# Performance work log

Hardware: AMD Instinct MI355X
Metric: run time of the kernel (lower is better)

The kernel has to match this reference:

```python
import jax, jax.numpy as jnp
import numpy as np

DIM = 768
HEADS = 12
HEAD_DIM = DIM // HEADS
WS = 14  # window size
MLP = 3072
EPS = 1e-6
SCALE = HEAD_DIM ** -0.5
B, H, W = 4, 64, 64


def setup_inputs() -> dict:
    key = jax.random.key(0)
    ks = jax.random.split(key, 8)
    s = 0.02
    f32 = jnp.float32
    return {
        "hidden_states": jax.random.normal(ks[0], (B, DIM, H, W), f32),
        "ln1_w": jnp.ones((DIM,), f32),
        "ln1_b": jnp.zeros((DIM,), f32),
        "qkv_w": jax.random.normal(ks[1], (DIM, 3 * DIM), f32) * s,
        "qkv_b": jnp.zeros((3 * DIM,), f32),
        "proj_w": jax.random.normal(ks[2], (DIM, DIM), f32) * s,
        "proj_b": jnp.zeros((DIM,), f32),
        "rel_pos_h": jax.random.normal(ks[3], (2 * WS - 1, HEAD_DIM), f32) * s,
        "rel_pos_w": jax.random.normal(ks[4], (2 * WS - 1, HEAD_DIM), f32) * s,
        "ln2_w": jnp.ones((DIM,), f32),
        "ln2_b": jnp.zeros((DIM,), f32),
        "fc1_w": jax.random.normal(ks[5], (DIM, MLP), f32) * s,
        "fc1_b": jnp.zeros((MLP,), f32),
        "fc2_w": jax.random.normal(ks[6], (MLP, DIM), f32) * s,
        "fc2_b": jnp.zeros((DIM,), f32),
    }


def _layer_norm(x, w, b):
    mu = jnp.mean(x, axis=-1, keepdims=True)
    var = jnp.mean(jnp.square(x - mu), axis=-1, keepdims=True)
    return (x - mu) * jax.lax.rsqrt(var + EPS) * w + b


def _get_rel_pos(size, rel_pos):
    # q_size == k_size == WS, rel_pos already has 2*WS-1 rows -> pure gather
    coords = jnp.arange(size)[:, None] - jnp.arange(size)[None, :] + (size - 1)
    return rel_pos[coords]  # (size, size, head_dim)


def _attention(x, qkv_w, qkv_b, proj_w, proj_b, rel_pos_h, rel_pos_w):
    nb, h, w, c = x.shape  # windows batch, WS, WS, DIM
    n = h * w
    qkv = x.reshape(nb, n, c) @ qkv_w + qkv_b  # (nb, n, 3*DIM)
    qkv = qkv.reshape(nb, n, 3, HEADS, HEAD_DIM).transpose(2, 0, 3, 1, 4)
    qkv = qkv.reshape(3, nb * HEADS, n, HEAD_DIM)
    q, k, v = qkv[0], qkv[1], qkv[2]
    attn = jnp.einsum('bqc,bkc->bqk', q * SCALE, k)  # (nb*HEADS, n, n)
    # decomposed relative position bias
    Rh = _get_rel_pos(h, rel_pos_h)  # (h, h, hd)
    Rw = _get_rel_pos(w, rel_pos_w)  # (w, w, hd)
    rq = q.reshape(-1, h, w, HEAD_DIM)
    rel_h = jnp.einsum('bhwc,hkc->bhwk', rq, Rh)
    rel_w = jnp.einsum('bhwc,wkc->bhwk', rq, Rw)
    attn = (attn.reshape(-1, h, w, h, w)
            + rel_h[:, :, :, :, None]
            + rel_w[:, :, :, None, :]).reshape(-1, n, n)
    attn = jax.nn.softmax(attn, axis=-1)
    out = attn @ v  # (nb*HEADS, n, hd)
    out = out.reshape(nb, HEADS, h, w, HEAD_DIM).transpose(0, 2, 3, 1, 4)
    out = out.reshape(nb, h, w, c)
    return out @ proj_w + proj_b


def reference(hidden_states, ln1_w, ln1_b, qkv_w, qkv_b, proj_w, proj_b,
              rel_pos_h, rel_pos_w, ln2_w, ln2_b, fc1_w, fc1_b, fc2_w, fc2_b):
    x = hidden_states.transpose(0, 2, 3, 1)  # NCHW -> NHWC
    b, h, w, c = x.shape
    shortcut = x
    x = _layer_norm(x, ln1_w, ln1_b)
    # window partition with padding
    ph = (WS - h % WS) % WS
    pw = (WS - w % WS) % WS
    x = jnp.pad(x, ((0, 0), (0, ph), (0, pw), (0, 0)))
    hp, wp = h + ph, w + pw
    x = x.reshape(b, hp // WS, WS, wp // WS, WS, c).transpose(0, 1, 3, 2, 4, 5)
    windows = x.reshape(-1, WS, WS, c)
    windows = _attention(windows, qkv_w, qkv_b, proj_w, proj_b, rel_pos_h, rel_pos_w)
    # window unpartition + crop
    x = windows.reshape(b, hp // WS, wp // WS, WS, WS, c).transpose(0, 1, 3, 2, 4, 5)
    x = x.reshape(b, hp, wp, c)[:, :h, :w, :]
    x = shortcut + x
    y = _layer_norm(x, ln2_w, ln2_b)
    y = jax.nn.gelu(y @ fc1_w + fc1_b, approximate=False) @ fc2_w + fc2_b
    x = x + y
    return x.transpose(0, 3, 1, 2)  # back to NCHW
```

## Files before the change

### kernel.cpp

```cpp
#include <hip/hip_runtime.h>
#include <cstdint>
#include <cstddef>

#define NIMG   4
#define GRIDSZ 64
#define CH     768
#define NHEAD  12
#define WSZ    14
#define NWINS  100
#define NTOK   196
#define MWIN   19600
#define MREAL  16384
#define MLPC   3072
#define QKSCALE 0.125f

#define KSTR 72
#define VSTR 216
#define PSTR 40

typedef unsigned short u16;
typedef __attribute__((ext_vector_type(8))) short bf16x8;
typedef __attribute__((ext_vector_type(4))) float f32x4;

__device__ __forceinline__ float b2f(u16 u) {
  uint32_t x = (uint32_t)u << 16; float f; __builtin_memcpy(&f, &x, 4); return f;
}
__device__ __forceinline__ u16 f2b(float f) {
  uint32_t x; __builtin_memcpy(&x, &f, 4);
  x += 0x7fffu + ((x >> 16) & 1u);
  return (u16)(x >> 16);
}

__device__ __forceinline__ float fast_gelu(float x) {
  float z  = x * 0.70710678118654752440f;
  float az = fabsf(z);
  float t  = 1.0f / (1.0f + 0.3275911f * az);
  float poly = ((((1.061405429f * t - 1.453152027f) * t + 1.421413741f) * t
                 - 0.284496736f) * t + 0.254829592f) * t;
  float e  = __expf(-az * az);
  float erfv = copysignf(1.0f - poly * e, z);
  return 0.5f * x * (1.0f + erfv);
}

__device__ __forceinline__ void gl_lds16(const u16* g, u16* l) {
  __builtin_amdgcn_global_load_lds(
      (const __attribute__((address_space(1))) unsigned int*)g,
      (__attribute__((address_space(3))) unsigned int*)l, 16, 0, 0);
}

__global__ __launch_bounds__(256) void k_nchw2nhwc(const float* __restrict__ in,
                                                   float* __restrict__ out) {
  __shared__ float tile[32][33];
  int b  = blockIdx.z;
  int g0 = blockIdx.x * 32;
  int c0 = blockIdx.y * 32;
  int tx = threadIdx.x, ty = threadIdx.y;
  const float* ip = in + (size_t)b * CH * 4096;
  float* op = out + (size_t)b * 4096 * CH;
#pragma unroll
  for (int k = 0; k < 32; k += 8)
    tile[ty + k][tx] = ip[(size_t)(c0 + ty + k) * 4096 + g0 + tx];
  __syncthreads();
#pragma unroll
  for (int k = 0; k < 32; k += 8)
    op[(size_t)(g0 + ty + k) * CH + c0 + tx] = tile[tx][ty + k];
}

__global__ __launch_bounds__(256) void k_nhwc2nchw(const float* __restrict__ in,
                                                   float* __restrict__ out) {
  __shared__ float tile[32][33];
  int b  = blockIdx.z;
  int g0 = blockIdx.x * 32;
  int c0 = blockIdx.y * 32;
  int tx = threadIdx.x, ty = threadIdx.y;
  const float* ip = in + (size_t)b * 4096 * CH;
  float* op = out + (size_t)b * CH * 4096;
#pragma unroll
  for (int k = 0; k < 32; k += 8)
    tile[ty + k][tx] = ip[(size_t)(g0 + ty + k) * CH + c0 + tx];
  __syncthreads();
#pragma unroll
  for (int k = 0; k < 32; k += 8)
    op[(size_t)(c0 + ty + k) * 4096 + g0 + tx] = tile[tx][ty + k];
}

__global__ __launch_bounds__(256) void k_wt(const float* __restrict__ in,
                                            u16* __restrict__ out,
                                            int K, int N) {
  __shared__ float t[32][33];
  int n0 = blockIdx.x * 32, k0 = blockIdx.y * 32;
  int tx = threadIdx.x, ty = threadIdx.y;
#pragma unroll
  for (int k = 0; k < 32; k += 8)
    t[ty + k][tx] = in[(size_t)(k0 + ty + k) * N + n0 + tx];
  __syncthreads();
#pragma unroll
  for (int k = 0; k < 32; k += 8)
    out[(size_t)(n0 + ty + k) * K + k0 + tx] = f2b(t[tx][ty + k]);
}

__global__ __launch_bounds__(256) void k_ln(const float* __restrict__ x,
                                            const float* __restrict__ wt,
                                            const float* __restrict__ bs,
                                            u16* __restrict__ y,
                                            int window_mode) {
  int wid = threadIdx.x >> 6, lane = threadIdx.x & 63;
  int row = blockIdx.x * 4 + wid;
  const float* xp = x + (size_t)row * CH;
  float v[12];
#pragma unroll
  for (int k = 0; k < 6; k++) {
    float2 f2 = *(const float2*)&xp[k * 128 + lane * 2];
    v[2 * k] = f2.x; v[2 * k + 1] = f2.y;
  }
  float s = 0.f;
#pragma unroll
  for (int k = 0; k < 12; k++) s += v[k];
#pragma unroll
  for (int off = 32; off > 0; off >>= 1) s += __shfl_xor(s, off, 64);
  float mu = s * (1.0f / 768.0f);
  float vs = 0.f;
#pragma unroll
  for (int k = 0; k < 12; k++) { float d = v[k] - mu; vs += d * d; }
#pragma unroll
  for (int off = 32; off > 0; off >>= 1) vs += __shfl_xor(vs, off, 64);
  float rs = rsqrtf(vs * (1.0f / 768.0f) + 1e-6f);
  int orow = row;
  if (window_mode) {
    int b = row >> 12, hw = row & 4095;
    int h = hw >> 6, wc = hw & 63;
    orow = (b * 25 + (h / WSZ) * 5 + (wc / WSZ)) * NTOK + (h % WSZ) * WSZ + (wc % WSZ);
  }
  u16* yp = y + (size_t)orow * CH;
#pragma unroll
  for (int k = 0; k < 6; k++) {
    int c = k * 128 + lane * 2;
    float2 w2 = *(const float2*)&wt[c];
    float2 b2 = *(const float2*)&bs[c];
    ushort2 st = make_ushort2(f2b((v[2 * k] - mu) * rs * w2.x + b2.x),
                              f2b((v[2 * k + 1] - mu) * rs * w2.y + b2.y));
    *(ushort2*)&yp[c] = st;
  }
}

__device__ __forceinline__ void gemm_epilogue_row(
    const f32x4* accrow, int row, int colbase, int N,
    const float* __restrict__ bias, void* __restrict__ Cv,
    u16* __restrict__ Vt, int act, int mode, int row0, int M) {
  if (row >= M) return;
  size_t gbase = 0;
  bool valid = true;
  int wloc = 0, tok = 0;
  if (mode == 2) {
    int rowa = row + row0;
    int widx = rowa / NTOK, tt = rowa % NTOK;
    int b = widx / 25, wq = widx % 25;
    int h = (wq / 5) * WSZ + tt / WSZ;
    int w = (wq % 5) * WSZ + tt % WSZ;
    valid = (h < GRIDSZ) && (w < GRIDSZ);
    gbase = valid ? ((size_t)((b * GRIDSZ + h) * GRIDSZ + w)) * CH : 0;
  }
  if (mode == 3) { wloc = row / NTOK; tok = row - wloc * NTOK; }
#pragma unroll
  for (int ni = 0; ni < 4; ni++) {
    int colb = colbase + ni * 16;
    float4 b4 = *(const float4*)&bias[colb];
    float v[4] = {accrow[ni][0] + b4.x, accrow[ni][1] + b4.y,
                  accrow[ni][2] + b4.z, accrow[ni][3] + b4.w};
    if (act == 1) {
#pragma unroll
      for (int r2 = 0; r2 < 4; r2++) v[r2] = fast_gelu(v[r2]);
    }
    if (mode == 0) {
      ushort4 st = make_ushort4(f2b(v[0]), f2b(v[1]), f2b(v[2]), f2b(v[3]));
      *(ushort4*)((u16*)Cv + (size_t)row * N + colb) = st;
    } else if (mode == 1) {
      float4* p = (float4*)((float*)Cv + (size_t)row * N + colb);
      float4 o = *p;
      o.x += v[0]; o.y += v[1]; o.z += v[2]; o.w += v[3];
      *p = o;
    } else if (mode == 2) {
      if (valid) {
        float4* p = (float4*)((float*)Cv + gbase + colb);
        float4 o = *p;
        o.x += v[0]; o.y += v[1]; o.z += v[2]; o.w += v[3];
        *p = o;
      }
    } else {
      if (colb < 1536) {
        ushort4 st = make_ushort4(f2b(v[0]), f2b(v[1]), f2b(v[2]), f2b(v[3]));
        *(ushort4*)((u16*)Cv + (size_t)row * N + colb) = st;
      } else {
        int vv = colb - 1536, hd = vv >> 6, d = vv & 63;
        u16* vp = Vt + ((size_t)(wloc * NHEAD + hd) * 64 + d) * VSTR + tok;
#pragma unroll
        for (int r2 = 0; r2 < 4; r2++) vp[(size_t)r2 * VSTR] = f2b(v[r2]);
      }
    }
  }
}

__global__ __launch_bounds__(256, 3) void k_gemm_mfma(const u16* __restrict__ A,
                                                      const u16* __restrict__ BT,
                                                      const float* __restrict__ bias,
                                                      void* __restrict__ Cv,
                                                      u16* __restrict__ Vt,
                                                      int M, int N, int K,
                                                      int act, int mode, int row0) {
  __shared__ u16 As[3][128 * 32];
  __shared__ u16 Bs[3][128 * 32];
  int tid  = threadIdx.x;
  int lane = tid & 63, wave = tid >> 6;

  int gx   = gridDim.x, gy = gridDim.y;
  int nwg  = gx * gy;
  int orig = blockIdx.y * gx + blockIdx.x;
  int q = nwg >> 3, r = nwg & 7;
  int xcd = orig & 7, idx = orig >> 3;
  int wgid = (xcd < r ? xcd * (q + 1) : r * (q + 1) + (xcd - r) * q) + idx;

  int GM = 3145728 / (128 * K * 2);
  if (GM < 2) GM = 2;
  if (GM > gy) GM = gy;
  int gsz   = GM * gx;
  int grp   = wgid / gsz;
  int first = grp * GM;
  int gm    = gy - first; if (gm > GM) gm = GM;
  int loc   = wgid - grp * gsz;
  int bm    = first + loc % gm;
  int bn    = loc / gm;

  int wm = (wave & 1) * 64, wn = (wave >> 1) * 64;
  int l15 = lane & 15, quad = lane >> 4;
  int xq = (quad ^ ((l15 >> 1) & 3)) * 8;

  f32x4 acc[4][4];
#pragma unroll
  for (int i = 0; i < 4; i++)
#pragma unroll
    for (int j = 0; j < 4; j++) acc[i][j] = (f32x4){0.f, 0.f, 0.f, 0.f};

  const u16* Atile = A + (size_t)bm * 128 * K;
  const u16* Btile = BT + (size_t)bn * 128 * K;

  const u16* ga[2];
  const u16* gb[2];
#pragma unroll
  for (int i = 0; i < 2; ++i) {
    int c_ = i * 256 + wave * 64 + lane;
    int row_ = c_ >> 2, gs_ = (c_ & 3) ^ ((c_ >> 3) & 3);
    ga[i] = Atile + (size_t)row_ * K + gs_ * 8;
    gb[i] = Btile + (size_t)row_ * K + gs_ * 8;
  }

  const int nk = K >> 5;

#define STAGE(slot)                                                          \
  do {                                                                       \
    _Pragma("unroll")                                                        \
    for (int i = 0; i < 2; ++i) {                                            \
      gl_lds16(ga[i], &As[(slot)][(i * 256 + wave * 64) * 8]);               \
      ga[i] += 32;                                                           \
      gl_lds16(gb[i], &Bs[(slot)][(i * 256 + wave * 64) * 8]);               \
      gb[i] += 32;                                                           \
    }                                                                        \
  } while (0)

#define COMPUTE(slot)                                                        \
  do {                                                                       \
    bf16x8 af[4], bfv[4];                                                    \
    _Pragma("unroll")                                                        \
    for (int mi = 0; mi < 4; mi++)                                           \
      af[mi] = *(const bf16x8*)&As[(slot)][(wm + mi * 16 + l15) * 32 + xq];  \
    _Pragma("unroll")                                                        \
    for (int ni = 0; ni < 4; ni++)                                           \
      bfv[ni] = *(const bf16x8*)&Bs[(slot)][(wn + ni * 16 + l15) * 32 + xq]; \
    _Pragma("unroll")                                                        \
    for (int mi = 0; mi < 4; mi++)                                           \
      _Pragma("unroll")                                                      \
      for (int ni = 0; ni < 4; ni++)                                         \
        acc[mi][ni] = __builtin_amdgcn_mfma_f32_16x16x32_bf16(               \
            bfv[ni], af[mi], acc[mi][ni], 0, 0, 0);                          \
  } while (0)

#define WAITL                                                                \
  do {                                                                       \
    asm volatile("s_waitcnt vmcnt(4)" ::: "memory");                         \
    __builtin_amdgcn_s_barrier();                                            \
  } while (0)

  STAGE(0);
  STAGE(1);

  for (int g = 0; g < nk - 3; g += 3) {
    WAITL; STAGE(2); COMPUTE(0);
    WAITL; STAGE(0); COMPUTE(1);
    WAITL; STAGE(1); COMPUTE(2);
  }
  WAITL; STAGE(2); COMPUTE(0);
  WAITL;           COMPUTE(1);
  asm volatile("s_waitcnt vmcnt(0)" ::: "memory");
  __builtin_amdgcn_s_barrier();
  COMPUTE(2);

#undef STAGE
#undef COMPUTE
#undef WAITL

#pragma unroll
  for (int mi = 0; mi < 4; mi++) {
    int row = bm * 128 + wm + mi * 16 + l15;
    int colbase = bn * 128 + wn + quad * 4;
    gemm_epilogue_row(acc[mi], row, colbase, N, bias, Cv, Vt, act, mode, row0, M);
  }
}

__global__ __launch_bounds__(256) void k_relbias(const u16* __restrict__ qkv,
                                                 const float* __restrict__ rel_h,
                                                 const float* __restrict__ rel_w,
                                                 u16* __restrict__ rhg,
                                                 u16* __restrict__ rwg,
                                                 int nrows) {
  int idx = blockIdx.x * 256 + threadIdx.x;
  if (idx >= nrows * NHEAD) return;
  int head = idx % NHEAD, row = idx / NHEAD;
  int wloc = row / NTOK, tok = row - wloc * NTOK;
  const u16* qp = qkv + (size_t)row * (3 * CH) + head * 64;
  float q[64];
#pragma unroll
  for (int d = 0; d < 64; d += 4) {
    ushort4 u4 = *(const ushort4*)(qp + d);
    q[d] = b2f(u4.x); q[d + 1] = b2f(u4.y); q[d + 2] = b2f(u4.z); q[d + 3] = b2f(u4.w);
  }
  int hq = tok / WSZ, wq = tok % WSZ;
  size_t obase = ((size_t)(wloc * NHEAD + head) * NTOK + tok) * 16;
  for (int kk = 0; kk < WSZ; kk++) {
    const float* rh = rel_h + (size_t)(hq - kk + WSZ - 1) * 64;
    const float* rw = rel_w + (size_t)(wq - kk + WSZ - 1) * 64;
    float sh = 0.0f, sw = 0.0f;
#pragma unroll
    for (int d = 0; d < 64; d++) { sh += q[d] * rh[d]; sw += q[d] * rw[d]; }
    rhg[obase + kk] = f2b(sh);
    rwg[obase + kk] = f2b(sw);
  }
}

__global__ __launch_bounds__(256) void k_attn_mfma(const u16* __restrict__ qkv,
                                                   const u16* __restrict__ Vt,
                                                   const u16* __restrict__ rhg,
                                                   const u16* __restrict__ rwg,
                                                   u16* __restrict__ out,
                                                   int win0) {
  __shared__ u16 Ks[NTOK * KSTR];
  __shared__ u16 Vs[64 * VSTR];
  __shared__ u16 Ps[4][16 * PSTR];
  __shared__ u16 RhL[NTOK * 16];
  __shared__ u16 RwL[NTOK * 16];
  int head = blockIdx.x, wloc = blockIdx.y;
  int tid = threadIdx.x, lane = tid & 63, wave = tid >> 6;
  int l15 = lane & 15, quad = lane >> 4;
  const u16* qbase = qkv + (size_t)wloc * NTOK * (3 * CH) + head * 64;

  for (int c = tid; c < NTOK * 8; c += 256) {
    int tok = c >> 3, part = c & 7;
    uint4 v = *(const uint4*)(qbase + (size_t)tok * (3 * CH) + CH + part * 8);
    *(uint4*)&Ks[tok * KSTR + part * 8] = v;
  }
  {
    const uint4* rhp4 = (const uint4*)(rhg + ((size_t)(wloc * NHEAD + head) * NTOK) * 16);
    const uint4* rwp4 = (const uint4*)(rwg + ((size_t)(wloc * NHEAD + head) * NTOK) * 16);
    for (int c = tid; c < NTOK * 2; c += 256) {
      ((uint4*)RhL)[c] = rhp4[c];
      ((uint4*)RwL)[c] = rwp4[c];
    }
  }
  const u16* vb = Vt + (size_t)(wloc * NHEAD + head) * 64 * VSTR;
#pragma unroll
  for (int it = 0; it < 7; ++it) {
    int c = it * 256 + tid;
    if (c < 64 * VSTR / 8) gl_lds16(vb + (size_t)c * 8, Vs + ((size_t)it * 256 + wave * 64) * 8);
  }
  __syncthreads();

  int winabs = win0 + wloc;

  for (int t16 = wave; t16 < 13; t16 += 4) {
    int qtok = t16 * 16 + l15; if (qtok > NTOK - 1) qtok = NTOK - 1;
    bf16x8 aq0 = *(const bf16x8*)(qbase + (size_t)qtok * (3 * CH) + quad * 8);
    bf16x8 aq1 = *(const bf16x8*)(qbase + (size_t)qtok * (3 * CH) + 32 + quad * 8);

    f32x4 s[13];
#pragma unroll
    for (int ct = 0; ct < 13; ct++) s[ct] = (f32x4){0.f, 0.f, 0.f, 0.f};
#pragma unroll
    for (int ct = 0; ct < 13; ct++) {
      int ktok = ct * 16 + l15; if (ktok > NTOK - 1) ktok = NTOK - 1;
      bf16x8 bk0 = *(const bf16x8*)&Ks[ktok * KSTR + quad * 8];
      bf16x8 bk1 = *(const bf16x8*)&Ks[ktok * KSTR + 32 + quad * 8];
      s[ct] = __builtin_amdgcn_mfma_f32_16x16x32_bf16(aq0, bk0, s[ct], 0, 0, 0);
      s[ct] = __builtin_amdgcn_mfma_f32_16x16x32_bf16(aq1, bk1, s[ct], 0, 0, 0);
    }

    f32x4 o[4];
#pragma unroll
    for (int ni = 0; ni < 4; ni++) o[ni] = (f32x4){0.f, 0.f, 0.f, 0.f};
    float lsum[4] = {0.f, 0.f, 0.f, 0.f};
    int row0t = t16 * 16 + quad * 4;

#pragma unroll
    for (int cc = 0; cc < 7; ++cc) {
#pragma unroll
      for (int half = 0; half < 2; ++half) {
        int ct = cc * 2 + half;
        if (ct < 13) {
          int col = ct * 16 + l15;
          int jh = col / WSZ, jw = col - jh * WSZ;
          bool colok = col < NTOK;
#pragma unroll
          for (int r = 0; r < 4; r++) {
            int rowt = row0t + r; int rowc = rowt > NTOK - 1 ? NTOK - 1 : rowt;
            float bias = b2f(RhL[rowc * 16 + jh]) + b2f(RwL[rowc * 16 + jw]);
            float sv = s[ct][r] * QKSCALE + bias;
            float p = colok ? __expf(sv) : 0.f;
            lsum[r] += p;
            Ps[wave][(quad * 4 + r) * PSTR + half * 16 + l15] = f2b(p);
          }
        } else {
#pragma unroll
          for (int r = 0; r < 4; r++)
            Ps[wave][(quad * 4 + r) * PSTR + half * 16 + l15] = 0;
        }
      }
      bf16x8 pa = *(const bf16x8*)&Ps[wave][l15 * PSTR + quad * 8];
#pragma unroll
      for (int ni = 0; ni < 4; ni++) {
        bf16x8 bv = *(const bf16x8*)&Vs[(ni * 16 + l15) * VSTR + cc * 32 + quad * 8];
        o[ni] = __builtin_amdgcn_mfma_f32_16x16x32_bf16(pa, bv, o[ni], 0, 0, 0);
      }
    }

#pragma unroll
    for (int r = 0; r < 4; r++) {
#pragma unroll
      for (int m = 1; m < 16; m <<= 1) lsum[r] += __shfl_xor(lsum[r], m, 64);
    }

#pragma unroll
    for (int r = 0; r < 4; r++) {
      int rowt = row0t + r;
      if (rowt < NTOK) {
        float inv = 1.0f / lsum[r];
        u16* op = out + ((size_t)winabs * NTOK + rowt) * CH + head * 64;
#pragma unroll
        for (int ni = 0; ni < 4; ni++) op[ni * 16 + l15] = f2b(o[ni][r] * inv);
      }
    }
  }
}

extern "C" void kernel_launch(void* const* d_in, const int* in_sizes, int n_in,
                              void* d_out, int out_size, void* d_ws, size_t ws_size,
                              hipStream_t stream) {
  const float* hidden = (const float*)d_in[0];
  const float* ln1_w  = (const float*)d_in[1];
  const float* ln1_b  = (const float*)d_in[2];
  const float* qkv_w  = (const float*)d_in[3];
  const float* qkv_b  = (const float*)d_in[4];
  const float* proj_w = (const float*)d_in[5];
  const float* proj_b = (const float*)d_in[6];
  const float* rel_h  = (const float*)d_in[7];
  const float* rel_w  = (const float*)d_in[8];
  const float* ln2_w  = (const float*)d_in[9];
  const float* ln2_b  = (const float*)d_in[10];
  const float* fc1_w  = (const float*)d_in[11];
  const float* fc1_b  = (const float*)d_in[12];
  const float* fc2_w  = (const float*)d_in[13];
  const float* fc2_b  = (const float*)d_in[14];
  float* out = (float*)d_out;

  char* ws = (char*)d_ws;
  float* x_nhwc = (float*)ws;
  u16*   R1     = (u16*)(ws + 50331648);
  u16*   qkvT   = (u16*)(ws + 80437248);
  u16*   projT  = qkvT + (size_t)2304 * 768;
  u16*   fc1T   = projT + (size_t)768 * 768;
  u16*   fc2T   = fc1T + (size_t)3072 * 768;
  u16*   R2     = fc2T + (size_t)768 * 3072;
  size_t used   = (size_t)80437248 + 14155776;
  size_t r2e    = ws_size > used ? (ws_size - used) >> 1 : 0;

  const size_t PW_QKV = (size_t)NTOK * 3 * CH;
  const size_t PW_VT  = (size_t)NHEAD * 64 * VSTR;
  const size_t PW_RB  = (size_t)NHEAD * NTOK * 16;
  const size_t perwin = PW_QKV + PW_VT + 2 * PW_RB;
  size_t wc_s = r2e / perwin;
  int Wc = wc_s >= NWINS ? NWINS : (int)wc_s;
  if (Wc < 1) Wc = 1;
  size_t rc_s = (r2e / MLPC / 128) * 128;
  int Rc = rc_s >= MREAL ? MREAL : (int)rc_s;
  if (Rc < 128) Rc = 128;

  u16* Vt  = R2 + (size_t)Wc * PW_QKV;
  u16* rhg = Vt + (size_t)Wc * PW_VT;
  u16* rwg = rhg + (size_t)Wc * PW_RB;

  k_wt<<<dim3(72, 24), dim3(32, 8), 0, stream>>>(qkv_w, qkvT, CH, 3 * CH);
  k_wt<<<dim3(24, 24), dim3(32, 8), 0, stream>>>(proj_w, projT, CH, CH);
  k_wt<<<dim3(96, 24), dim3(32, 8), 0, stream>>>(fc1_w, fc1T, CH, MLPC);
  k_wt<<<dim3(24, 96), dim3(32, 8), 0, stream>>>(fc2_w, fc2T, MLPC, CH);

  hipMemsetAsync(R1, 0, (size_t)MWIN * CH * sizeof(u16), stream);

  k_nchw2nhwc<<<dim3(128, 24, NIMG), dim3(32, 8), 0, stream>>>(hidden, x_nhwc);
  k_ln<<<MREAL / 4, 256, 0, stream>>>(x_nhwc, ln1_w, ln1_b, R1, 1);
  for (int w0 = 0; w0 < NWINS; w0 += Wc) {
    int wc = NWINS - w0 < Wc ? NWINS - w0 : Wc;
    int Mc = wc * NTOK;
    k_gemm_mfma<<<dim3(18, (Mc + 127) / 128), 256, 0, stream>>>(
        R1 + (size_t)w0 * NTOK * CH, qkvT, qkv_b, R2, Vt,
        Mc, 3 * CH, CH, 0, 3, 0);
    k_relbias<<<(Mc * NHEAD + 255) / 256, 256, 0, stream>>>(
        R2, rel_h, rel_w, rhg, rwg, Mc);
    k_attn_mfma<<<dim3(NHEAD, wc), 256, 0, stream>>>(
        R2, Vt, rhg, rwg, R1, w0);
  }
  k_gemm_mfma<<<dim3(6, (MWIN + 127) / 128), 256, 0, stream>>>(
      R1, projT, proj_b, x_nhwc, nullptr, MWIN, CH, CH, 0, 2, 0);
  k_ln<<<MREAL / 4, 256, 0, stream>>>(x_nhwc, ln2_w, ln2_b, R1, 0);
  for (int r0 = 0; r0 < MREAL; r0 += Rc) {
    int rc = MREAL - r0 < Rc ? MREAL - r0 : Rc;
    k_gemm_mfma<<<dim3(24, (rc + 127) / 128), 256, 0, stream>>>(
        R1 + (size_t)r0 * CH, fc1T, fc1_b, R2, nullptr, rc, MLPC, CH, 1, 0, 0);
    k_gemm_mfma<<<dim3(6, (rc + 127) / 128), 256, 0, stream>>>(
        R2, fc2T, fc2_b, x_nhwc + (size_t)r0 * CH, nullptr, rc, CH, MLPC, 0, 1, 0);
  }
  k_nhwc2nchw<<<dim3(128, 24, NIMG), dim3(32, 8), 0, stream>>>(x_nhwc, out);
}
```

Before: 745.6 us.

## Add barrier-free per-wave-staged GEMM kernel for MLP fc1/fc2

Adds a new GEMM kernel in which each wave loads its own 64-row A and B slices into private LDS buffers with direct global-to-LDS copies. Wave-local data lets the double-buffered pipeline use only vmcnt/lgkmcnt waits, with no workgroup barriers. The MLP fc1 and fc2 GEMMs switch to this kernel. In exchange, A and B rows are duplicated across waves, which doubles global/L2 traffic and LDS footprint, so occupancy drops to 2 blocks per CU. The block-mapping code is moved into a shared helper.

```diff
diff --git a/kernel.cpp b/kernel.cpp
--- a/kernel.cpp
+++ b/kernel.cpp
@@ -200,6 +200,119 @@
   }
 }
 
+__device__ __forceinline__ void map_block(int K, int& bm, int& bn) {
+  int gx = gridDim.x, gy = gridDim.y;
+  int nwg = gx * gy;
+  int orig = blockIdx.y * gx + blockIdx.x;
+  int q = nwg >> 3, r = nwg & 7;
+  int xcd = orig & 7, idx = orig >> 3;
+  int wgid = (xcd < r ? xcd * (q + 1) : r * (q + 1) + (xcd - r) * q) + idx;
+  int GM = 3145728 / (128 * K * 2);
+  if (GM < 2) GM = 2;
+  if (GM > gy) GM = gy;
+  int gsz   = GM * gx;
+  int grp   = wgid / gsz;
+  int first = grp * GM;
+  int gm    = gy - first; if (gm > GM) gm = GM;
+  int loc   = wgid - grp * gsz;
+  bm = first + loc % gm;
+  bn = loc / gm;
+}
+
+__global__ __launch_bounds__(256, 2) void k_gemm_nb(const u16* __restrict__ A,
+                                                    const u16* __restrict__ BT,
+                                                    const float* __restrict__ bias,
+                                                    void* __restrict__ Cv,
+                                                    u16* __restrict__ Vt,
+                                                    int M, int N, int K,
+                                                    int act, int mode, int row0) {
+  __shared__ u16 Aw[4][2][64 * 32];
+  __shared__ u16 Bw[4][2][64 * 32];
+  int tid  = threadIdx.x;
+  int lane = tid & 63, wave = tid >> 6;
+
+  int bm, bn;
+  map_block(K, bm, bn);
+
+  int wm = (wave & 1) * 64, wn = (wave >> 1) * 64;
+  int l15 = lane & 15, quad = lane >> 4;
+  int xq = (quad ^ ((l15 >> 1) & 3)) * 8;
+
+  f32x4 acc[4][4];
+#pragma unroll
+  for (int i = 0; i < 4; i++)
+#pragma unroll
+    for (int j = 0; j < 4; j++) acc[i][j] = (f32x4){0.f, 0.f, 0.f, 0.f};
+
+  const u16* Atile = A + (size_t)(bm * 128 + wm) * K;
+  const u16* Btile = BT + (size_t)(bn * 128 + wn) * K;
+
+  const u16* ga[4];
+  const u16* gb[4];
+#pragma unroll
+  for (int i = 0; i < 4; ++i) {
+    int c_ = i * 64 + lane;
+    int row_ = c_ >> 2, gs_ = (c_ & 3) ^ ((c_ >> 3) & 3);
+    ga[i] = Atile + (size_t)row_ * K + gs_ * 8;
+    gb[i] = Btile + (size_t)row_ * K + gs_ * 8;
+  }
+
+  const int nk = K >> 5;
+
+#define STG(slot)                                                            \
+  do {                                                                       \
+    _Pragma("unroll")                                                        \
+    for (int i = 0; i < 4; ++i) {                                            \
+      gl_lds16(ga[i], &Aw[wave][(slot)][i * 512]);                           \
+      ga[i] += 32;                                                           \
+      gl_lds16(gb[i], &Bw[wave][(slot)][i * 512]);                           \
+      gb[i] += 32;                                                           \
+    }                                                                        \
+  } while (0)
+
+#define SLAB(slot, last)                                                     \
+  do {                                                                       \
+    if (last) asm volatile("s_waitcnt vmcnt(0)" ::: "memory");               \
+    else      asm volatile("s_waitcnt vmcnt(8)" ::: "memory");               \
+    bf16x8 af[4], bfv[4];                                                    \
+    _Pragma("unroll")                                                        \
+    for (int mi = 0; mi < 4; mi++)                                           \
+      af[mi] = *(const bf16x8*)&Aw[wave][(slot)][(mi * 16 + l15) * 32 + xq]; \
+    _Pragma("unroll")                                                        \
+    for (int ni = 0; ni < 4; ni++)                                           \
+      bfv[ni] = *(const bf16x8*)&Bw[wave][(slot)][(ni * 16 + l15) * 32 + xq];\
+    asm volatile("s_waitcnt lgkmcnt(0)" ::: "memory");                       \
+    __builtin_amdgcn_sched_barrier(0);                                       \
+    if (t2 < nk) STG(slot);   \
+    _Pragma("unroll")                                                        \
+    for (int mi = 0; mi < 4; mi++)                                           \
+      _Pragma("unroll")                                                      \
+      for (int ni = 0; ni < 4; ni++)                                         \
+        acc[mi][ni] = __builtin_amdgcn_mfma_f32_16x16x32_bf16(               \
+            bfv[ni], af[mi], acc[mi][ni], 0, 0, 0);                          \
+  } while (0)
+
+  STG(0);
+  STG(1);
+
+  for (int t = 0; t < nk; t += 2) {
+    int t2 = t + 2;
+    SLAB(0, false);
+    t2 = t + 3;
+    SLAB(1, t + 2 >= nk);
+  }
+
+#undef STG
+#undef SLAB
+
+#pragma unroll
+  for (int mi = 0; mi < 4; mi++) {
+    int row = bm * 128 + wm + mi * 16 + l15;
+    int colbase = bn * 128 + wn + quad * 4;
+    gemm_epilogue_row(acc[mi], row, colbase, N, bias, Cv, Vt, act, mode, row0, M);
+  }
+}
+
 __global__ __launch_bounds__(256, 3) void k_gemm_mfma(const u16* __restrict__ A,
                                                       const u16* __restrict__ BT,
                                                       const float* __restrict__ bias,
@@ -212,23 +325,8 @@
   int tid  = threadIdx.x;
   int lane = tid & 63, wave = tid >> 6;
 
-  int gx   = gridDim.x, gy = gridDim.y;
-  int nwg  = gx * gy;
-  int orig = blockIdx.y * gx + blockIdx.x;
-  int q = nwg >> 3, r = nwg & 7;
-  int xcd = orig & 7, idx = orig >> 3;
-  int wgid = (xcd < r ? xcd * (q + 1) : r * (q + 1) + (xcd - r) * q) + idx;
-
-  int GM = 3145728 / (128 * K * 2);
-  if (GM < 2) GM = 2;
-  if (GM > gy) GM = gy;
-  int gsz   = GM * gx;
-  int grp   = wgid / gsz;
-  int first = grp * GM;
-  int gm    = gy - first; if (gm > GM) gm = GM;
-  int loc   = wgid - grp * gsz;
-  int bm    = first + loc % gm;
-  int bn    = loc / gm;
+  int bm, bn;
+  map_block(K, bm, bn);
 
   int wm = (wave & 1) * 64, wn = (wave >> 1) * 64;
   int l15 = lane & 15, quad = lane >> 4;
@@ -529,9 +627,9 @@
   k_ln<<<MREAL / 4, 256, 0, stream>>>(x_nhwc, ln2_w, ln2_b, R1, 0);
   for (int r0 = 0; r0 < MREAL; r0 += Rc) {
     int rc = MREAL - r0 < Rc ? MREAL - r0 : Rc;
-    k_gemm_mfma<<<dim3(24, (rc + 127) / 128), 256, 0, stream>>>(
+    k_gemm_nb<<<dim3(24, (rc + 127) / 128), 256, 0, stream>>>(
         R1 + (size_t)r0 * CH, fc1T, fc1_b, R2, nullptr, rc, MLPC, CH, 1, 0, 0);
-    k_gemm_mfma<<<dim3(6, (rc + 127) / 128), 256, 0, stream>>>(
+    k_gemm_nb<<<dim3(6, (rc + 127) / 128), 256, 0, stream>>>(
         R2, fc2T, fc2_b, x_nhwc + (size_t)r0 * CH, nullptr, rc, CH, MLPC, 0, 1, 0);
   }
   k_nhwc2nchw<<<dim3(128, 24, NIMG), dim3(32, 8), 0, stream>>>(x_nhwc, out);
```

Result: slower. 827.4 us (+11.0%).
